# Optimization experiments

Measured on AMD Instinct MI355X. Metric: run time of the kernel, lower is better.

## Reference

```python
import jax, jax.numpy as jnp
import numpy as np
import math

D = 512      # d_model
HEADS = 16   # num_heads
HD = 32      # head_dim
WS = 7       # window_size
KS = 8       # patch_size
S = 4        # spectral_stride


def dct_basis(n):
    k = np.arange(n, dtype=np.float64)[:, None]
    i = np.arange(n, dtype=np.float64)[None, :]
    B = np.cos(np.pi * (i + 0.5) * k / n)
    B[0, :] *= 1.0 / np.sqrt(2.0)
    B = B * np.sqrt(2.0 / n)
    return jnp.asarray(B, dtype=jnp.float32)


def setup_inputs() -> dict:
    key = jax.random.key(0)
    ks = jax.random.split(key, 24)
    Bb, H, W = 4, 112, 112
    N = H * W
    w = lambda k, shape: jax.random.normal(k, shape, jnp.float32) * 0.02
    return {
        'tokens': jax.random.normal(ks[0], (Bb, N, D), jnp.float32),
        'patches': jax.random.normal(ks[1], (Bb, 3 * KS * KS, N), jnp.float32),
        'Wq': w(ks[2], (D, D)), 'bq': w(ks[3], (D,)),
        'Wk': w(ks[4], (D, D)), 'bk': w(ks[5], (D,)),
        'Wv': w(ks[6], (D, D)), 'bv': w(ks[7], (D,)),
        'Wo': w(ks[8], (D, D)), 'bo': w(ks[9], (D,)),
        'Wsp': w(ks[10], (3 * KS * KS, D)), 'bsp': w(ks[11], (D,)),
        'Wsq': w(ks[12], (D, D)), 'bsq': w(ks[13], (D,)),
        'Wsk': w(ks[14], (D, D)), 'bsk': w(ks[15], (D,)),
        'Wsv': w(ks[16], (D, D)), 'bsv': w(ks[17], (D,)),
        'Wso': w(ks[18], (D, D)), 'bso': w(ks[19], (D,)),
        'alpha': jnp.asarray(0.5, jnp.float32),
        'H': H, 'W': W,
    }


def reference(tokens, patches, Wq, bq, Wk, bk, Wv, bv, Wo, bo,
              Wsp, bsp, Wsq, bsq, Wsk, bsk, Wsv, bsv, Wso, bso,
              alpha, H, W):
    B, N, d = tokens.shape
    # ---- local windowed multi-head attention ----
    ws = WS
    pad_h = (-H) % ws
    pad_w = (-W) % ws
    x = tokens.reshape(B, H, W, d)
    if pad_h or pad_w:
        x = jnp.pad(x, ((0, 0), (0, pad_h), (0, pad_w), (0, 0)))
    Hp, Wp = H + pad_h, W + pad_w
    nh, nw_ = Hp // ws, Wp // ws
    xw = x.reshape(B, nh, ws, nw_, ws, d).transpose(0, 1, 3, 2, 4, 5)
    xw = xw.reshape(B * nh * nw_, ws * ws, d)  # (nw, 49, d)
    nw, L, _ = xw.shape
    q = (xw @ Wq + bq).reshape(nw, L, HEADS, HD)
    k = (xw @ Wk + bk).reshape(nw, L, HEADS, HD)
    v = (xw @ Wv + bv).reshape(nw, L, HEADS, HD)
    scale = 1.0 / math.sqrt(HD)
    attn = jax.nn.softmax(jnp.einsum('nqhd,nkhd->nhqk', q, k) * scale, axis=-1)
    o = jnp.einsum('nhqk,nkhd->nqhd', attn, v).reshape(nw, L, d)
    o = o @ Wo + bo
    o = o.reshape(B, nh, nw_, ws, ws, d).transpose(0, 1, 3, 2, 4, 5).reshape(B, Hp, Wp, d)
    sp_out = o[:, :H, :W, :].reshape(B, N, d)
    # ---- DCT on raw patches -> spectral descriptors ----
    Bm = dct_basis(KS)
    p = patches.reshape(B, 3, KS, KS, N)
    Fc = jnp.einsum('ij,bcjkn->bcikn', Bm, p)
    Fc = jnp.einsum('bcijn,jk->bcikn', Fc, Bm)  # right-multiply by Bm^T transposed back
    spec_desc = Fc.reshape(B, 3 * KS * KS, N).transpose(0, 2, 1) @ Wsp + bsp  # (B,N,d)
    # ---- strided global spectral attention + nearest upsample ----
    spec_hw = spec_desc.reshape(B, H, W, d)
    sd = spec_hw[:, ::S, ::S, :]
    Hs, Ws = sd.shape[1], sd.shape[2]
    sd = sd.reshape(B, Hs * Ws, d)
    qs = sd @ Wsq + bsq
    ks_ = sd @ Wsk + bsk
    vs = sd @ Wsv + bsv
    a = jax.nn.softmax(jnp.einsum('bqd,bkd->bqk', qs, ks_) / math.sqrt(d), axis=-1)
    so = jnp.einsum('bqk,bkd->bqd', a, vs) @ Wso + bso
    so = so.reshape(B, Hs, Ws, d)
    ri = (jnp.arange(H) * Hs) // H  # torch nearest: floor(i*in/out)
    ci = (jnp.arange(W) * Ws) // W
    spec_out = so[:, ri][:, :, ci].reshape(B, N, d)
    # ---- fuse + residual + layernorm (no affine) ----
    al = jax.nn.sigmoid(alpha)
    out = tokens + al * sp_out + (1.0 - al) * spec_out
    mu = out.mean(-1, keepdims=True)
    var = ((out - mu) ** 2).mean(-1, keepdims=True)
    return (out - mu) / jnp.sqrt(var + 1e-5)
```

## Files before the change

### kernel.cpp

```cpp
#include <hip/hip_runtime.h>

typedef unsigned short u16;
typedef __attribute__((ext_vector_type(4))) float f32x4;
typedef __attribute__((ext_vector_type(8))) short bf16x8;

#define AS1 __attribute__((address_space(1)))
#define AS3 __attribute__((address_space(3)))
#define GLL(gp, lp) __builtin_amdgcn_global_load_lds((const AS1 void*)(gp), (AS3 void*)(lp), 16, 0, 0)

__device__ __forceinline__ float b2f(u16 v) { return __uint_as_float(((unsigned)v) << 16); }
__device__ __forceinline__ u16 f2b(float f) {
  unsigned u = __float_as_uint(f);
  u += 0x7fffu + ((u >> 16) & 1u);
  return (u16)(u >> 16);
}
__device__ __forceinline__ unsigned pack2(float a, float b) {
  return (unsigned)f2b(a) | ((unsigned)f2b(b) << 16);
}
__device__ __forceinline__ float blo(unsigned u) { return __uint_as_float(u << 16); }
__device__ __forceinline__ float bhi(unsigned u) { return __uint_as_float(u & 0xffff0000u); }

__global__ __launch_bounds__(256, 5) void gemm_bt128(
    const u16* __restrict__ A, int lda,
    const u16* __restrict__ Bt, int ldb,
    const float* __restrict__ bias, void* __restrict__ Cv, int ldc,
    int M, int N, int K, int c_bf16)
{
  __shared__ __align__(16) u16 ldsA[128 * 64];
  __shared__ __align__(16) u16 ldsB[128 * 64];
  int tid = threadIdx.x;
  int wid = tid >> 6, lane = tid & 63;

  int nbx = gridDim.x;
  int lin = blockIdx.y * nbx + blockIdx.x;
  int nwg = nbx * gridDim.y;
  int qc = nwg >> 3, rc = nwg & 7;
  int xcd = lin & 7, pos = lin >> 3;
  int nlin = (xcd < rc ? xcd * (qc + 1) : rc * (qc + 1) + (xcd - rc) * qc) + pos;
  int bx = nlin % nbx, by = nlin / nbx;

  int row0 = by << 7;
  int col0 = bx << 7;
  int wr = (wid >> 1) << 6, wc = (wid & 1) << 6;

  const u16* pA[4];
  const u16* pB[4];
  int ldso[4];
#pragma unroll
  for (int q = 0; q < 4; ++q) {
    int inst = (wid << 2) + q;
    int o = (inst << 10) + (lane << 4);
    int r = o >> 7;
    int cs = (o >> 4) & 7;
    int cl = cs ^ (r & 7);
    int ar = row0 + r; ar = ar < M ? ar : M - 1;
    int br = col0 + r; br = br < N ? br : N - 1;
    pA[q] = A + (size_t)ar * lda + (cl << 3);
    pB[q] = Bt + (size_t)br * ldb + (cl << 3);
    ldso[q] = inst << 9;
  }

  f32x4 acc[4][4];
#pragma unroll
  for (int i = 0; i < 4; ++i)
#pragma unroll
    for (int j = 0; j < 4; ++j) { f32x4 z = {0.f, 0.f, 0.f, 0.f}; acc[i][j] = z; }

  int nt = K >> 6;
  for (int t = 0; t < nt; ++t) {
#pragma unroll
    for (int q = 0; q < 4; ++q) {
      GLL(pA[q], ldsA + ldso[q]);
      GLL(pB[q], ldsB + ldso[q]);
      pA[q] += 64; pB[q] += 64;
    }
    __syncthreads();
#pragma unroll
    for (int kk = 0; kk < 2; ++kk) {
      bf16x8 af[4], bg[4];
#pragma unroll
      for (int mi = 0; mi < 4; ++mi) {
        int r = wr + (mi << 4) + (lane & 15);
        int cs = ((kk << 2) + (lane >> 4)) ^ (r & 7);
        af[mi] = *(const bf16x8*)(ldsA + (r << 6) + (cs << 3));
      }
#pragma unroll
      for (int ni = 0; ni < 4; ++ni) {
        int r = wc + (ni << 4) + (lane & 15);
        int cs = ((kk << 2) + (lane >> 4)) ^ (r & 7);
        bg[ni] = *(const bf16x8*)(ldsB + (r << 6) + (cs << 3));
      }
#pragma unroll
      for (int mi = 0; mi < 4; ++mi)
#pragma unroll
        for (int ni = 0; ni < 4; ++ni)
          acc[mi][ni] = __builtin_amdgcn_mfma_f32_16x16x32_bf16(af[mi], bg[ni], acc[mi][ni], 0, 0, 0);
    }
    __syncthreads();
  }

#pragma unroll
  for (int mi = 0; mi < 4; ++mi) {
    int rb = row0 + wr + (mi << 4) + ((lane >> 4) << 2);
#pragma unroll
    for (int ni = 0; ni < 4; ++ni) {
      int c = col0 + wc + (ni << 4) + (lane & 15);
      float bv = (bias && c < N) ? bias[c] : 0.f;
#pragma unroll
      for (int j = 0; j < 4; ++j) {
        int r = rb + j;
        if (r < M && c < N) {
          float v = acc[mi][ni][j] + bv;
          if (c_bf16) ((u16*)Cv)[(size_t)r * ldc + c] = f2b(v);
          else ((float*)Cv)[(size_t)r * ldc + c] = v;
        }
      }
    }
  }
}

__global__ __launch_bounds__(256, 6) void gemm_bt(
    const u16* __restrict__ A, int lda, long sAb,
    const u16* __restrict__ Bt, int ldb, long sBb,
    const float* __restrict__ bias, void* __restrict__ Cv, int ldc, long sCb,
    int M, int N, int K, int c_bf16)
{
  __shared__ __align__(16) u16 ldsA[128 * 64];
  __shared__ __align__(16) u16 ldsB[64 * 64];
  int tid = threadIdx.x;
  int wid = tid >> 6, lane = tid & 63;

  int nbx = gridDim.x;
  int lin = blockIdx.y * nbx + blockIdx.x;
  int nwg = nbx * gridDim.y;
  int qc = nwg >> 3, rc = nwg & 7;
  int xcd = lin & 7, pos = lin >> 3;
  int nlin = (xcd < rc ? xcd * (qc + 1) : rc * (qc + 1) + (xcd - rc) * qc) + pos;
  int bx = nlin % nbx, by = nlin / nbx;

  int row0 = by << 7;
  int col0 = bx << 6;
  int bz = blockIdx.z;
  A += (size_t)bz * sAb;
  Bt += (size_t)bz * sBb;
  int wr = (wid >> 1) << 6, wc = (wid & 1) << 5;

  const u16* pA[4];
  const u16* pB[2];
  int ldsoA[4], ldsoB[2];
#pragma unroll
  for (int q = 0; q < 4; ++q) {
    int inst = (wid << 2) + q;
    int o = (inst << 10) + (lane << 4);
    int r = o >> 7;
    int cs = (o >> 4) & 7;
    int cl = cs ^ (r & 7);
    int ar = row0 + r; ar = ar < M ? ar : M - 1;
    pA[q] = A + (size_t)ar * lda + (cl << 3);
    ldsoA[q] = inst << 9;
  }
#pragma unroll
  for (int q = 0; q < 2; ++q) {
    int inst = (wid << 1) + q;
    int o = (inst << 10) + (lane << 4);
    int r = o >> 7;
    int cs = (o >> 4) & 7;
    int cl = cs ^ (r & 7);
    int br = col0 + r; br = br < N ? br : N - 1;
    pB[q] = Bt + (size_t)br * ldb + (cl << 3);
    ldsoB[q] = inst << 9;
  }

  f32x4 acc[4][2];
#pragma unroll
  for (int i = 0; i < 4; ++i)
#pragma unroll
    for (int j = 0; j < 2; ++j) { f32x4 z = {0.f, 0.f, 0.f, 0.f}; acc[i][j] = z; }

  int nt = K >> 6;
  for (int t = 0; t < nt; ++t) {
#pragma unroll
    for (int q = 0; q < 4; ++q) { GLL(pA[q], ldsA + ldsoA[q]); pA[q] += 64; }
#pragma unroll
    for (int q = 0; q < 2; ++q) { GLL(pB[q], ldsB + ldsoB[q]); pB[q] += 64; }
    __syncthreads();
#pragma unroll
    for (int kk = 0; kk < 2; ++kk) {
      bf16x8 af[4], bg[2];
#pragma unroll
      for (int mi = 0; mi < 4; ++mi) {
        int r = wr + (mi << 4) + (lane & 15);
        int cs = ((kk << 2) + (lane >> 4)) ^ (r & 7);
        af[mi] = *(const bf16x8*)(ldsA + (r << 6) + (cs << 3));
      }
#pragma unroll
      for (int ni = 0; ni < 2; ++ni) {
        int r = wc + (ni << 4) + (lane & 15);
        int cs = ((kk << 2) + (lane >> 4)) ^ (r & 7);
        bg[ni] = *(const bf16x8*)(ldsB + (r << 6) + (cs << 3));
      }
#pragma unroll
      for (int mi = 0; mi < 4; ++mi)
#pragma unroll
        for (int ni = 0; ni < 2; ++ni)
          acc[mi][ni] = __builtin_amdgcn_mfma_f32_16x16x32_bf16(af[mi], bg[ni], acc[mi][ni], 0, 0, 0);
    }
    __syncthreads();
  }

#pragma unroll
  for (int mi = 0; mi < 4; ++mi) {
    int rb = row0 + wr + (mi << 4) + ((lane >> 4) << 2);
#pragma unroll
    for (int ni = 0; ni < 2; ++ni) {
      int c = col0 + wc + (ni << 4) + (lane & 15);
      float bv = (bias && c < N) ? bias[c] : 0.f;
#pragma unroll
      for (int j = 0; j < 4; ++j) {
        int r = rb + j;
        if (r < M && c < N) {
          float v = acc[mi][ni][j] + bv;
          if (c_bf16) ((u16*)Cv)[(size_t)bz * sCb + (size_t)r * ldc + c] = f2b(v);
          else ((float*)Cv)[(size_t)bz * sCb + (size_t)r * ldc + c] = v;
        }
      }
    }
  }
}

__global__ __launch_bounds__(256, 2) void win_attn_mfma(const u16* __restrict__ qkv, u16* __restrict__ oat)
{
  __shared__ __align__(16) u16 Pl[4][64 * 72];
  __shared__ __align__(16) u16 Vtl[4][32 * 72];
  int tid = threadIdx.x;
  int wid = tid >> 6, lane = tid & 63;
  int lm = lane & 15, lg = lane >> 4;
  int w = blockIdx.x;
  int b = w >> 8, wh = (w >> 4) & 15, ww = w & 15;
  int rowbase = (wh * 7) * 112 + ww * 7;
  u16* P = Pl[wid];
  u16* Vt = Vtl[wid];
  const u16* base = qkv + (size_t)b * 12544 * 1536;
  u16* ob = oat + (size_t)b * 12544 * 512;
  const float scale = 0.17677669529663687f;

  for (int hh = 0; hh < 4; ++hh) {
    int h = wid * 4 + hh;
    bf16x8 Qf[4], Kf[4];
#pragma unroll
    for (int mi = 0; mi < 4; ++mi) {
      int i = mi * 16 + lm; i = i < 49 ? i : 48;
      int q7 = (i * 147) >> 10;
      int n = rowbase + q7 * 112 + (i - q7 * 7);
      const u16* rp = base + (size_t)n * 1536 + h * 32 + lg * 8;
      Qf[mi] = *(const bf16x8*)(rp);
      Kf[mi] = *(const bf16x8*)(rp + 512);
    }
    {
      int j = lane;
      if (j < 49) {
        int q7 = (j * 147) >> 10;
        int n = rowbase + q7 * 112 + (j - q7 * 7);
        const uint4* vp = (const uint4*)(base + (size_t)n * 1536 + 1024 + h * 32);
#pragma unroll
        for (int t = 0; t < 4; ++t) {
          uint4 u = vp[t];
          Vt[(t * 8 + 0) * 72 + j] = (u16)(u.x & 0xffff); Vt[(t * 8 + 1) * 72 + j] = (u16)(u.x >> 16);
          Vt[(t * 8 + 2) * 72 + j] = (u16)(u.y & 0xffff); Vt[(t * 8 + 3) * 72 + j] = (u16)(u.y >> 16);
          Vt[(t * 8 + 4) * 72 + j] = (u16)(u.z & 0xffff); Vt[(t * 8 + 5) * 72 + j] = (u16)(u.z >> 16);
          Vt[(t * 8 + 6) * 72 + j] = (u16)(u.w & 0xffff); Vt[(t * 8 + 7) * 72 + j] = (u16)(u.w >> 16);
        }
      } else {
#pragma unroll
        for (int d = 0; d < 32; ++d) Vt[d * 72 + j] = 0;
      }
    }
    f32x4 S[4][4];
#pragma unroll
    for (int mi = 0; mi < 4; ++mi)
#pragma unroll
      for (int nj = 0; nj < 4; ++nj) { f32x4 z = {0.f, 0.f, 0.f, 0.f}; S[mi][nj] = z; }
#pragma unroll
    for (int mi = 0; mi < 4; ++mi)
#pragma unroll
      for (int nj = 0; nj < 4; ++nj)
        S[mi][nj] = __builtin_amdgcn_mfma_f32_16x16x32_bf16(Qf[mi], Kf[nj], S[mi][nj], 0, 0, 0);
    float invv[4][4];
#pragma unroll
    for (int mi = 0; mi < 4; ++mi) {
#pragma unroll
      for (int reg = 0; reg < 4; ++reg) {
        float v0 = S[mi][0][reg], v1 = S[mi][1][reg], v2 = S[mi][2][reg], v3 = S[mi][3][reg];
        if (lm) v3 = -1e30f;
        float m = fmaxf(fmaxf(v0, v1), fmaxf(v2, v3));
#pragma unroll
        for (int o = 1; o < 16; o <<= 1) m = fmaxf(m, __shfl_xor(m, o));
        float e0 = __expf((v0 - m) * scale);
        float e1 = __expf((v1 - m) * scale);
        float e2 = __expf((v2 - m) * scale);
        float e3 = lm ? 0.f : __expf((v3 - m) * scale);
        float s = e0 + e1 + e2 + e3;
#pragma unroll
        for (int o = 1; o < 16; o <<= 1) s += __shfl_xor(s, o);
        invv[mi][reg] = 1.f / s;
        int r = mi * 16 + lg * 4 + reg;
        P[r * 72 + lm] = f2b(e0);
        P[r * 72 + 16 + lm] = f2b(e1);
        P[r * 72 + 32 + lm] = f2b(e2);
        P[r * 72 + 48 + lm] = f2b(e3);
      }
    }
    bf16x8 Vf[2][2];
#pragma unroll
    for (int dt = 0; dt < 2; ++dt) {
      Vf[dt][0] = *(const bf16x8*)(Vt + (dt * 16 + lm) * 72 + lg * 8);
      Vf[dt][1] = *(const bf16x8*)(Vt + (dt * 16 + lm) * 72 + 32 + lg * 8);
    }
    f32x4 O[4][2];
#pragma unroll
    for (int mi = 0; mi < 4; ++mi)
#pragma unroll
      for (int dt = 0; dt < 2; ++dt) { f32x4 z = {0.f, 0.f, 0.f, 0.f}; O[mi][dt] = z; }
#pragma unroll
    for (int mi = 0; mi < 4; ++mi) {
      bf16x8 Pf0 = *(const bf16x8*)(P + (mi * 16 + lm) * 72 + lg * 8);
      bf16x8 Pf1 = *(const bf16x8*)(P + (mi * 16 + lm) * 72 + 32 + lg * 8);
#pragma unroll
      for (int dt = 0; dt < 2; ++dt) {
        O[mi][dt] = __builtin_amdgcn_mfma_f32_16x16x32_bf16(Pf0, Vf[dt][0], O[mi][dt], 0, 0, 0);
        O[mi][dt] = __builtin_amdgcn_mfma_f32_16x16x32_bf16(Pf1, Vf[dt][1], O[mi][dt], 0, 0, 0);
      }
    }
#pragma unroll
    for (int mi = 0; mi < 4; ++mi)
#pragma unroll
      for (int reg = 0; reg < 4; ++reg) {
        int i = mi * 16 + lg * 4 + reg;
        if (i < 49) {
          int q7 = (i * 147) >> 10;
          int n = rowbase + q7 * 112 + (i - q7 * 7);
          float iv = invv[mi][reg];
          u16* op = ob + (size_t)n * 512 + h * 32 + lm;
          op[0] = f2b(O[mi][0][reg] * iv);
          op[16] = f2b(O[mi][1][reg] * iv);
        }
      }
  }
}

__global__ __launch_bounds__(192) void dct_f2(const float* __restrict__ patches, u16* __restrict__ F2)
{
  __shared__ float pv[192];
  __shared__ float Bm[64];
  int blk = blockIdx.x;
  int b = blk / 784, rem = blk % 784;
  int n = ((rem / 28) * 4) * 112 + (rem % 28) * 4;
  int t = threadIdx.x;
  if (t < 64) {
    int k = t >> 3, ii = t & 7;
    float v = cosf(3.14159265358979323846f * (ii + 0.5f) * (float)k * 0.125f) * 0.5f;
    if (k == 0) v *= 0.70710678118654752f;
    Bm[t] = v;
  }
  pv[t] = patches[((size_t)b * 192 + t) * 12544 + n];
  __syncthreads();
  int c = t >> 6, fi = (t >> 3) & 7, fk = t & 7;
  float acc = 0.f;
#pragma unroll
  for (int mm = 0; mm < 8; ++mm) {
    float g = 0.f;
#pragma unroll
    for (int jj = 0; jj < 8; ++jj) g += pv[c * 64 + mm * 8 + jj] * Bm[jj * 8 + fk];
    acc += Bm[fi * 8 + mm] * g;
  }
  F2[(size_t)blk * 192 + t] = f2b(acc);
}

__global__ __launch_bounds__(256) void spec_softmax(const float* __restrict__ S, u16* __restrict__ P)
{
  __shared__ float red[4];
  int row = blockIdx.x;
  const float* sr = S + (size_t)row * 784;
  u16* pr = P + (size_t)row * 832;
  int t = threadIdx.x;
  int lane = t & 63, wid = t >> 6;
  float v0 = sr[t];
  float v1 = sr[t + 256];
  float v2 = (t < 272) ? sr[t + 512] : -1e30f;
  float m = fmaxf(fmaxf(v0, v1), v2);
#pragma unroll
  for (int ofs = 32; ofs > 0; ofs >>= 1) m = fmaxf(m, __shfl_xor(m, ofs));
  if (lane == 0) red[wid] = m;
  __syncthreads();
  m = fmaxf(fmaxf(red[0], red[1]), fmaxf(red[2], red[3]));
  __syncthreads();
  const float scale = 0.044194173824159216f;
  float e0 = __expf((v0 - m) * scale);
  float e1 = __expf((v1 - m) * scale);
  float e2 = (t < 272) ? __expf((v2 - m) * scale) : 0.f;
  float sum = e0 + e1 + e2;
#pragma unroll
  for (int ofs = 32; ofs > 0; ofs >>= 1) sum += __shfl_xor(sum, ofs);
  if (lane == 0) red[wid] = sum;
  __syncthreads();
  sum = red[0] + red[1] + red[2] + red[3];
  float inv = 1.f / sum;
  pr[t] = f2b(e0 * inv);
  pr[t + 256] = f2b(e1 * inv);
  if (t < 272) pr[t + 512] = f2b(e2 * inv);
  else if (t < 320) pr[t + 512] = 0;
}

__global__ __launch_bounds__(256) void transV(const u16* __restrict__ qkvs, u16* __restrict__ Vt)
{
  int idx = blockIdx.x * 256 + threadIdx.x;
  int k = idx % 832;
  int rest = idx / 832;
  int n = rest % 512, b = rest / 512;
  u16 v = 0;
  if (k < 784) v = qkvs[((size_t)(b * 784 + k)) * 1536 + 1024 + n];
  Vt[idx] = v;
}

__global__ __launch_bounds__(256) void combine_ln(
    const float* __restrict__ tokens, const u16* __restrict__ sp,
    const float* __restrict__ so, const float* __restrict__ alpha,
    float* __restrict__ out)
{
  int nidx = blockIdx.x;
  int b = nidx / 12544, pos = nidx % 12544;
  int i = pos / 112, j = pos % 112;
  const float* tr = tokens + (size_t)nidx * 512;
  const u16* sr = sp + (size_t)nidx * 512;
  const float* qr = so + (size_t)(b * 784 + (i >> 2) * 28 + (j >> 2)) * 512;
  float al = 1.f / (1.f + __expf(-alpha[0]));
  float be = 1.f - al;
  int t = threadIdx.x;
  float x0 = tr[t] + al * b2f(sr[t]) + be * qr[t];
  float x1 = tr[t + 256] + al * b2f(sr[t + 256]) + be * qr[t + 256];
  float s = x0 + x1, ss = x0 * x0 + x1 * x1;
#pragma unroll
  for (int ofs = 32; ofs > 0; ofs >>= 1) { s += __shfl_xor(s, ofs); ss += __shfl_xor(ss, ofs); }
  __shared__ float rs[4], rq[4];
  int lane = t & 63, wid = t >> 6;
  if (lane == 0) { rs[wid] = s; rq[wid] = ss; }
  __syncthreads();
  s = rs[0] + rs[1] + rs[2] + rs[3];
  ss = rq[0] + rq[1] + rq[2] + rq[3];
  float mu = s * 0.001953125f;
  float var = ss * 0.001953125f - mu * mu;
  float rstd = rsqrtf(var + 1e-5f);
  float* orow = out + (size_t)nidx * 512;
  orow[t] = (x0 - mu) * rstd;
  orow[t + 256] = (x1 - mu) * rstd;
}

__global__ __launch_bounds__(256) void transT(const float* __restrict__ src, u16* __restrict__ dst, int K, int Nc)
{
  int idx = blockIdx.x * 256 + threadIdx.x;
  if (idx >= K * Nc) return;
  int nn = idx / K, kk = idx % K;
  dst[idx] = f2b(src[(size_t)kk * Nc + nn]);
}

__global__ __launch_bounds__(256) void cvtbf(const float* __restrict__ src, u16* __restrict__ dst)
{
  size_t i = ((size_t)blockIdx.x * 256 + threadIdx.x) * 4;
  float4 v = *(const float4*)(src + i);
  uint2 u;
  u.x = pack2(v.x, v.y);
  u.y = pack2(v.z, v.w);
  *(uint2*)(dst + i) = u;
}

__global__ __launch_bounds__(256) void stack_bias(
    const float* bq_, const float* bk_, const float* bv_,
    const float* bsq_, const float* bsk_, const float* bsv_,
    float* bqkv, float* bsqkv)
{
  int i = blockIdx.x * 256 + threadIdx.x;
  if (i >= 1536) return;
  int r = i & 511;
  bqkv[i]  = (i < 512) ? bq_[r]  : (i < 1024) ? bk_[r]  : bv_[r];
  bsqkv[i] = (i < 512) ? bsq_[r] : (i < 1024) ? bsk_[r] : bsv_[r];
}

extern "C" void kernel_launch(void* const* d_in, const int* in_sizes, int n_in,
                              void* d_out, int out_size, void* d_ws, size_t ws_size,
                              hipStream_t stream) {
  (void)in_sizes; (void)n_in; (void)out_size; (void)ws_size;
  const float* tokens = (const float*)d_in[0];
  const float* patches = (const float*)d_in[1];
  const float* Wq  = (const float*)d_in[2];
  const float* bq  = (const float*)d_in[3];
  const float* Wk  = (const float*)d_in[4];
  const float* bk  = (const float*)d_in[5];
  const float* Wv  = (const float*)d_in[6];
  const float* bv  = (const float*)d_in[7];
  const float* Wo  = (const float*)d_in[8];
  const float* bo  = (const float*)d_in[9];
  const float* Wsp = (const float*)d_in[10];
  const float* bsp = (const float*)d_in[11];
  const float* Wsq = (const float*)d_in[12];
  const float* bsq = (const float*)d_in[13];
  const float* Wsk = (const float*)d_in[14];
  const float* bsk = (const float*)d_in[15];
  const float* Wsv = (const float*)d_in[16];
  const float* bsv = (const float*)d_in[17];
  const float* Wso = (const float*)d_in[18];
  const float* bso = (const float*)d_in[19];
  const float* alpha = (const float*)d_in[20];
  float* out = (float*)d_out;

  char* ws = (char*)d_ws;
  u16* tokbf  = (u16*)ws;
  u16* qkv    = (u16*)(ws + 51380224);
  char* pp    = ws + 51380224 + 154140672;
  u16* WqkvT  = (u16*)pp; pp += 1572864;
  u16* WoT    = (u16*)pp; pp += 524288;
  u16* WsqkvT = (u16*)pp; pp += 1572864;
  u16* WsoT   = (u16*)pp; pp += 524288;
  u16* WspT   = (u16*)pp; pp += 196608;
  float* bqkv = (float*)pp; pp += 6144;
  float* bsqkv= (float*)pp; pp += 6144;
  u16* F2b    = (u16*)pp; pp += 1204224;
  u16* sd     = (u16*)pp; pp += 3211264;
  u16* qkvs   = (u16*)pp; pp += 9633792;
  u16* sopre  = (u16*)pp; pp += 3211264;
  float* sofin= (float*)pp; pp += 6422528;

  float* Sbuf = (float*)tokbf;
  u16* Pbuf   = (u16*)(ws + 9834496);
  u16* Vt     = (u16*)(ws + 9834496 + 5218304);

  cvtbf<<<25088, 256, 0, stream>>>(tokens, tokbf);
  transT<<<1024, 256, 0, stream>>>(Wq, WqkvT, 512, 512);
  transT<<<1024, 256, 0, stream>>>(Wk, WqkvT + 262144, 512, 512);
  transT<<<1024, 256, 0, stream>>>(Wv, WqkvT + 524288, 512, 512);
  transT<<<1024, 256, 0, stream>>>(Wo, WoT, 512, 512);
  transT<<<1024, 256, 0, stream>>>(Wsq, WsqkvT, 512, 512);
  transT<<<1024, 256, 0, stream>>>(Wsk, WsqkvT + 262144, 512, 512);
  transT<<<1024, 256, 0, stream>>>(Wsv, WsqkvT + 524288, 512, 512);
  transT<<<1024, 256, 0, stream>>>(Wso, WsoT, 512, 512);
  transT<<<384, 256, 0, stream>>>(Wsp, WspT, 192, 512);
  stack_bias<<<6, 256, 0, stream>>>(bq, bk, bv, bsq, bsk, bsv, bqkv, bsqkv);

  gemm_bt128<<<dim3(12, 392), 256, 0, stream>>>(tokbf, 512, WqkvT, 512, bqkv, qkv, 1536, 50176, 1536, 512, 1);
  win_attn_mfma<<<1024, 256, 0, stream>>>(qkv, tokbf);
  gemm_bt128<<<dim3(4, 392), 256, 0, stream>>>(tokbf, 512, WoT, 512, bo, qkv, 512, 50176, 512, 512, 1);

  dct_f2<<<3136, 192, 0, stream>>>(patches, F2b);
  gemm_bt<<<dim3(8, 25), 256, 0, stream>>>(F2b, 192, 0, WspT, 192, 0, bsp, sd, 512, 0, 3136, 512, 192, 1);
  gemm_bt<<<dim3(24, 25), 256, 0, stream>>>(sd, 512, 0, WsqkvT, 512, 0, bsqkv, qkvs, 1536, 0, 3136, 1536, 512, 1);
  gemm_bt<<<dim3(13, 7, 4), 256, 0, stream>>>(qkvs, 1536, (long)784 * 1536, qkvs + 512, 1536, (long)784 * 1536,
                                              nullptr, Sbuf, 784, (long)784 * 784, 784, 784, 512, 0);
  spec_softmax<<<3136, 256, 0, stream>>>(Sbuf, Pbuf);
  transV<<<6656, 256, 0, stream>>>(qkvs, Vt);
  gemm_bt<<<dim3(8, 7, 4), 256, 0, stream>>>(Pbuf, 832, (long)784 * 832, Vt, 832, (long)512 * 832,
                                             nullptr, sopre, 512, (long)784 * 512, 784, 512, 832, 1);
  gemm_bt<<<dim3(8, 25), 256, 0, stream>>>(sopre, 512, 0, WsoT, 512, 0, bso, sofin, 512, 0, 3136, 512, 512, 0);

  combine_ln<<<50176, 256, 0, stream>>>(tokens, qkv, sofin, alpha, out);
}
```

Measured before the change: 543.2 us.

## Replace LDS-staged big GEMM with direct-global MFMA loads; tile weight transposes

The large QKV and output-projection GEMMs drop LDS staging via global_load_lds and instead load bf16x8 MFMA fragments straight from global memory into registers each 32-wide k step. This removes the LDS traffic and both barriers per k-tile, but every wave now re-fetches its A and B rows from global/L2 without sharing across the workgroup, and the loads are short 16-byte strided accesses per row. Separately, the weight-transpose kernel now goes through a padded 64x64 LDS tile so that both reads and writes are coalesced, replacing the strided gather.

```diff
diff --git a/kernel.cpp b/kernel.cpp
--- a/kernel.cpp
+++ b/kernel.cpp
@@ -20,16 +20,15 @@
 __device__ __forceinline__ float blo(unsigned u) { return __uint_as_float(u << 16); }
 __device__ __forceinline__ float bhi(unsigned u) { return __uint_as_float(u & 0xffff0000u); }
 
-__global__ __launch_bounds__(256, 5) void gemm_bt128(
+__global__ __launch_bounds__(256) void gemm_direct(
     const u16* __restrict__ A, int lda,
     const u16* __restrict__ Bt, int ldb,
     const float* __restrict__ bias, void* __restrict__ Cv, int ldc,
     int M, int N, int K, int c_bf16)
 {
-  __shared__ __align__(16) u16 ldsA[128 * 64];
-  __shared__ __align__(16) u16 ldsB[128 * 64];
   int tid = threadIdx.x;
   int wid = tid >> 6, lane = tid & 63;
+  int lm = lane & 15, lg = lane >> 4;
 
   int nbx = gridDim.x;
   int lin = blockIdx.y * nbx + blockIdx.x;
@@ -39,25 +38,20 @@
   int nlin = (xcd < rc ? xcd * (qc + 1) : rc * (qc + 1) + (xcd - rc) * qc) + pos;
   int bx = nlin % nbx, by = nlin / nbx;
 
-  int row0 = by << 7;
-  int col0 = bx << 7;
-  int wr = (wid >> 1) << 6, wc = (wid & 1) << 6;
-
-  const u16* pA[4];
-  const u16* pB[4];
-  int ldso[4];
-#pragma unroll
-  for (int q = 0; q < 4; ++q) {
-    int inst = (wid << 2) + q;
-    int o = (inst << 10) + (lane << 4);
-    int r = o >> 7;
-    int cs = (o >> 4) & 7;
-    int cl = cs ^ (r & 7);
-    int ar = row0 + r; ar = ar < M ? ar : M - 1;
-    int br = col0 + r; br = br < N ? br : N - 1;
-    pA[q] = A + (size_t)ar * lda + (cl << 3);
-    pB[q] = Bt + (size_t)br * ldb + (cl << 3);
-    ldso[q] = inst << 9;
+  int row0 = (by << 7) + ((wid >> 1) << 6);
+  int col0 = (bx << 7) + ((wid & 1) << 6);
+
+  const u16* pa[4];
+  const u16* pb[4];
+#pragma unroll
+  for (int mi = 0; mi < 4; ++mi) {
+    int r = row0 + mi * 16 + lm; r = r < M ? r : M - 1;
+    pa[mi] = A + (size_t)r * lda + lg * 8;
+  }
+#pragma unroll
+  for (int ni = 0; ni < 4; ++ni) {
+    int c = col0 + ni * 16 + lm; c = c < N ? c : N - 1;
+    pb[ni] = Bt + (size_t)c * ldb + lg * 8;
   }
 
   f32x4 acc[4][4];
@@ -66,45 +60,25 @@
 #pragma unroll
     for (int j = 0; j < 4; ++j) { f32x4 z = {0.f, 0.f, 0.f, 0.f}; acc[i][j] = z; }
 
-  int nt = K >> 6;
-  for (int t = 0; t < nt; ++t) {
-#pragma unroll
-    for (int q = 0; q < 4; ++q) {
-      GLL(pA[q], ldsA + ldso[q]);
-      GLL(pB[q], ldsB + ldso[q]);
-      pA[q] += 64; pB[q] += 64;
-    }
-    __syncthreads();
-#pragma unroll
-    for (int kk = 0; kk < 2; ++kk) {
-      bf16x8 af[4], bg[4];
-#pragma unroll
-      for (int mi = 0; mi < 4; ++mi) {
-        int r = wr + (mi << 4) + (lane & 15);
-        int cs = ((kk << 2) + (lane >> 4)) ^ (r & 7);
-        af[mi] = *(const bf16x8*)(ldsA + (r << 6) + (cs << 3));
-      }
-#pragma unroll
-      for (int ni = 0; ni < 4; ++ni) {
-        int r = wc + (ni << 4) + (lane & 15);
-        int cs = ((kk << 2) + (lane >> 4)) ^ (r & 7);
-        bg[ni] = *(const bf16x8*)(ldsB + (r << 6) + (cs << 3));
-      }
-#pragma unroll
-      for (int mi = 0; mi < 4; ++mi)
-#pragma unroll
-        for (int ni = 0; ni < 4; ++ni)
-          acc[mi][ni] = __builtin_amdgcn_mfma_f32_16x16x32_bf16(af[mi], bg[ni], acc[mi][ni], 0, 0, 0);
-    }
-    __syncthreads();
+  for (int kt = 0; kt < K; kt += 32) {
+    bf16x8 af[4], bg[4];
+#pragma unroll
+    for (int mi = 0; mi < 4; ++mi) { af[mi] = *(const bf16x8*)(pa[mi]); pa[mi] += 32; }
+#pragma unroll
+    for (int ni = 0; ni < 4; ++ni) { bg[ni] = *(const bf16x8*)(pb[ni]); pb[ni] += 32; }
+#pragma unroll
+    for (int mi = 0; mi < 4; ++mi)
+#pragma unroll
+      for (int ni = 0; ni < 4; ++ni)
+        acc[mi][ni] = __builtin_amdgcn_mfma_f32_16x16x32_bf16(af[mi], bg[ni], acc[mi][ni], 0, 0, 0);
   }
 
 #pragma unroll
   for (int mi = 0; mi < 4; ++mi) {
-    int rb = row0 + wr + (mi << 4) + ((lane >> 4) << 2);
+    int rb = row0 + (mi << 4) + (lg << 2);
 #pragma unroll
     for (int ni = 0; ni < 4; ++ni) {
-      int c = col0 + wc + (ni << 4) + (lane & 15);
+      int c = col0 + (ni << 4) + lm;
       float bv = (bias && c < N) ? bias[c] : 0.f;
 #pragma unroll
       for (int j = 0; j < 4; ++j) {
@@ -457,10 +431,20 @@
 
 __global__ __launch_bounds__(256) void transT(const float* __restrict__ src, u16* __restrict__ dst, int K, int Nc)
 {
-  int idx = blockIdx.x * 256 + threadIdx.x;
-  if (idx >= K * Nc) return;
-  int nn = idx / K, kk = idx % K;
-  dst[idx] = f2b(src[(size_t)kk * Nc + nn]);
+  __shared__ float tile[64][65];
+  int tk0 = blockIdx.y << 6, tn0 = blockIdx.x << 6;
+  int j = threadIdx.x & 63, i4 = threadIdx.x >> 6;
+#pragma unroll
+  for (int i = i4; i < 64; i += 4) {
+    int k = tk0 + i, n = tn0 + j;
+    tile[i][j] = (k < K && n < Nc) ? src[(size_t)k * Nc + n] : 0.f;
+  }
+  __syncthreads();
+#pragma unroll
+  for (int i = i4; i < 64; i += 4) {
+    int n = tn0 + i, k = tk0 + j;
+    if (n < Nc && k < K) dst[(size_t)n * K + k] = f2b(tile[j][i]);
+  }
 }
 
 __global__ __launch_bounds__(256) void cvtbf(const float* __restrict__ src, u16* __restrict__ dst)
@@ -534,20 +518,20 @@
   u16* Vt     = (u16*)(ws + 9834496 + 5218304);
 
   cvtbf<<<25088, 256, 0, stream>>>(tokens, tokbf);
-  transT<<<1024, 256, 0, stream>>>(Wq, WqkvT, 512, 512);
-  transT<<<1024, 256, 0, stream>>>(Wk, WqkvT + 262144, 512, 512);
-  transT<<<1024, 256, 0, stream>>>(Wv, WqkvT + 524288, 512, 512);
-  transT<<<1024, 256, 0, stream>>>(Wo, WoT, 512, 512);
-  transT<<<1024, 256, 0, stream>>>(Wsq, WsqkvT, 512, 512);
-  transT<<<1024, 256, 0, stream>>>(Wsk, WsqkvT + 262144, 512, 512);
-  transT<<<1024, 256, 0, stream>>>(Wsv, WsqkvT + 524288, 512, 512);
-  transT<<<1024, 256, 0, stream>>>(Wso, WsoT, 512, 512);
-  transT<<<384, 256, 0, stream>>>(Wsp, WspT, 192, 512);
+  transT<<<dim3(8, 8), 256, 0, stream>>>(Wq, WqkvT, 512, 512);
+  transT<<<dim3(8, 8), 256, 0, stream>>>(Wk, WqkvT + 262144, 512, 512);
+  transT<<<dim3(8, 8), 256, 0, stream>>>(Wv, WqkvT + 524288, 512, 512);
+  transT<<<dim3(8, 8), 256, 0, stream>>>(Wo, WoT, 512, 512);
+  transT<<<dim3(8, 8), 256, 0, stream>>>(Wsq, WsqkvT, 512, 512);
+  transT<<<dim3(8, 8), 256, 0, stream>>>(Wsk, WsqkvT + 262144, 512, 512);
+  transT<<<dim3(8, 8), 256, 0, stream>>>(Wsv, WsqkvT + 524288, 512, 512);
+  transT<<<dim3(8, 8), 256, 0, stream>>>(Wso, WsoT, 512, 512);
+  transT<<<dim3(8, 3), 256, 0, stream>>>(Wsp, WspT, 192, 512);
   stack_bias<<<6, 256, 0, stream>>>(bq, bk, bv, bsq, bsk, bsv, bqkv, bsqkv);
 
-  gemm_bt128<<<dim3(12, 392), 256, 0, stream>>>(tokbf, 512, WqkvT, 512, bqkv, qkv, 1536, 50176, 1536, 512, 1);
+  gemm_direct<<<dim3(12, 392), 256, 0, stream>>>(tokbf, 512, WqkvT, 512, bqkv, qkv, 1536, 50176, 1536, 512, 1);
   win_attn_mfma<<<1024, 256, 0, stream>>>(qkv, tokbf);
-  gemm_bt128<<<dim3(4, 392), 256, 0, stream>>>(tokbf, 512, WoT, 512, bo, qkv, 512, 50176, 512, 512, 1);
+  gemm_direct<<<dim3(4, 392), 256, 0, stream>>>(tokbf, 512, WoT, 512, bo, qkv, 512, 50176, 512, 512, 1);
 
   dct_f2<<<3136, 192, 0, stream>>>(patches, F2b);
   gemm_bt<<<dim3(8, 25), 256, 0, stream>>>(F2b, 192, 0, WspT, 192, 0, bsp, sd, 512, 0, 3136, 512, 192, 1);
```

Result: slower. 778.8 us (+43.4%).
